# Performance work log

Measured on AMD Instinct MI355X. Metric: run time of the kernel, lower is better.

## Reference

```python
import jax, jax.numpy as jnp
import numpy as np

N_NODES = 20000
T_STEPS = 8


def _layer_norm(x, g, b, eps=1e-5):
    mu = x.mean(-1, keepdims=True)
    var = ((x - mu) ** 2).mean(-1, keepdims=True)
    return (x - mu) * jax.lax.rsqrt(var + eps) * g + b


def _linear(x, W, b):
    # torch nn.Linear: x @ W.T + b, W is [out, in]
    return x @ W.T + b


def _gcn_conv(xw, norm, src, dst, b, n):
    # xw: pre-transformed features [N, H]; symmetric-normalized aggregation
    msg = xw[src] * norm[:, None]
    return jax.ops.segment_sum(msg, dst, num_segments=n) + b


def setup_inputs() -> dict:
    key = jax.random.key(0)
    ks = jax.random.split(key, 16)
    N, T, K, E, D, H, M = N_NODES, T_STEPS, 4000, 400000, 128, 128, 16
    s = 0.05
    return {
        "node_t": jax.random.randint(ks[0], (T, K), 0, N),
        "edge_index_t": jax.random.randint(ks[1], (T, 2, E), 0, N),
        "m": M,
        "emb": jax.random.normal(ks[2], (N, D), jnp.float32) * s,
        "convW1": jax.random.normal(ks[3], (H, D), jnp.float32) * s,
        "convb1": jnp.zeros((H,), jnp.float32),
        "convW2": jax.random.normal(ks[4], (H, H), jnp.float32) * s,
        "convb2": jnp.zeros((H,), jnp.float32),
        "tn_g": jnp.ones((H,), jnp.float32),
        "tn_b": jnp.zeros((H,), jnp.float32),
        "tok_w1": jax.random.normal(ks[5], (M, M), jnp.float32) * s,
        "tok_b1": jnp.zeros((M,), jnp.float32),
        "tok_w2": jax.random.normal(ks[6], (M, M), jnp.float32) * s,
        "tok_b2": jnp.zeros((M,), jnp.float32),
        "cn_g": jnp.ones((H,), jnp.float32),
        "cn_b": jnp.zeros((H,), jnp.float32),
        "ch_w1": jax.random.normal(ks[7], (H, H), jnp.float32) * s,
        "ch_b1": jnp.zeros((H,), jnp.float32),
        "ch_w2": jax.random.normal(ks[8], (H, H), jnp.float32) * s,
        "ch_b2": jnp.zeros((H,), jnp.float32),
    }


def reference(node_t, edge_index_t, m, emb, convW1, convb1, convW2, convb2,
              tn_g, tn_b, tok_w1, tok_b1, tok_w2, tok_b2,
              cn_g, cn_b, ch_w1, ch_b1, ch_w2, ch_b2):
    N = emb.shape[0]
    H = convW1.shape[0]
    gelu = lambda x: jax.nn.gelu(x, approximate=False)

    def mixer(x):  # x: [N, m, H]
        y = _layer_norm(x, tn_g, tn_b)
        y = jnp.swapaxes(y, 1, 2)                 # [N, H, m]
        y = _linear(gelu(_linear(y, tok_w1, tok_b1)), tok_w2, tok_b2)
        x = x + jnp.swapaxes(y, 1, 2)
        z = _layer_norm(x, cn_g, cn_b)
        z = _linear(gelu(_linear(z, ch_w1, ch_b1)), ch_w2, ch_b2)
        return x + z

    # conv linear transforms are per-node dense and constant w.r.t. step input emb
    xw1 = emb @ convW1.T                          # [N, H]
    self_loop = jnp.arange(N)

    def step(x_m, xs):
        node_i, edge_i = xs                        # [K], [2, E]
        x_m_new = mixer(x_m)
        x_new = x_m_new.mean(axis=1)               # FinalProcessLayer, discrete
        # GCN with self-loops and symmetric normalization
        src = jnp.concatenate([edge_i[0], self_loop])
        dst = jnp.concatenate([edge_i[1], self_loop])
        deg = jax.ops.segment_sum(jnp.ones_like(src, jnp.float32), dst,
                                  num_segments=N)
        dinv = jax.lax.rsqrt(jnp.maximum(deg, 1.0))
        norm = dinv[src] * dinv[dst]
        h = _gcn_conv(xw1, norm, src, dst, convb1, N)
        h = jax.nn.relu(h)
        h = _gcn_conv(h @ convW2.T, norm, src, dst, convb2, N)
        # zero rows of nodes present at this timestep (boolean-mask scatter)
        h = h.at[node_i].set(0.0)
        # slide window
        x_m = jnp.concatenate([x_m[:, 1:, :], h[:, None, :]], axis=1)
        return x_m, x_new

    x_m0 = jnp.zeros((N, m, H), jnp.float32)
    _, outs = jax.lax.scan(step, x_m0, (node_t, edge_index_t))
    return outs  # [T, N, H]
```

## Files before the change

kernel.cpp:

```cpp
#include <hip/hip_runtime.h>
#include <hip/hip_bf16.h>
#include <cstdint>
#include <cstddef>

#define NN 20000
#define HH 128
#define MM 16
#define KK 4000
#define EE 400000

typedef __attribute__((ext_vector_type(16))) float f16v;
typedef __attribute__((ext_vector_type(8))) short short8;
typedef __attribute__((ext_vector_type(4))) float f32x4;
typedef __attribute__((ext_vector_type(4), may_alias)) float f4ma;
typedef __attribute__((ext_vector_type(2), may_alias)) float f2ma;

__device__ __forceinline__ float gelu_f(float x) {
  return 0.5f * x * (1.0f + erff(x * 0.70710678118654752440f));
}

__device__ __forceinline__ short f2bf(float f) {
  union { float f; unsigned u; } v; v.f = f;
  unsigned u = v.u;
  unsigned r = (u + 0x7FFFu + ((u >> 16) & 1u)) >> 16;
  return (short)r;
}
__device__ __forceinline__ float bf2f(unsigned short s) {
  union { unsigned u; float f; } v; v.u = ((unsigned)s) << 16; return v.f;
}


__global__ void zero2_kernel(int* __restrict__ a, int* __restrict__ b, int n) {
  int i = blockIdx.x * 256 + threadIdx.x;
  if (i < n) { a[i] = 0; b[i] = 0; }
}

__global__ void count_kernel(const int* __restrict__ dst, int* __restrict__ cnt, int n) {
  int e = blockIdx.x * 256 + threadIdx.x;
  if (e < n) atomicAdd(&cnt[dst[e]], 1);
}

__global__ void dinv_kernel(const int* __restrict__ cnt, float* __restrict__ dinv, int n) {
  int i = blockIdx.x * 256 + threadIdx.x;
  if (i < n) dinv[i] = rsqrtf((float)(cnt[i] + 1));
}

__global__ void scan_kernel(const int* __restrict__ cnt, int* __restrict__ offs, int n) {
  __shared__ int sh[1024];
  __shared__ int carry_s;
  int tid = threadIdx.x;
  if (tid == 0) carry_s = 0;
  __syncthreads();
  for (int base = 0; base < n; base += 1024) {
    int i = base + tid;
    int v = (i < n) ? cnt[i] : 0;
    sh[tid] = v;
    __syncthreads();
    for (int off = 1; off < 1024; off <<= 1) {
      int t = (tid >= off) ? sh[tid - off] : 0;
      __syncthreads();
      sh[tid] += t;
      __syncthreads();
    }
    int carry = carry_s;
    if (i < n) offs[i] = carry + sh[tid] - v;
    __syncthreads();
    if (tid == 1023) carry_s = carry + sh[1023];
    __syncthreads();
  }
  if (tid == 0) offs[n] = carry_s;
}

__global__ void fillcsr_kernel(const int* __restrict__ esrc, const int* __restrict__ edst,
                               const int* __restrict__ offs, int* __restrict__ cursor,
                               const float* __restrict__ dinv,
                               int* __restrict__ csrc, float* __restrict__ cnorm, int n) {
  int e = blockIdx.x * 256 + threadIdx.x;
  if (e < n) {
    int s = esrc[e], d = edst[e];
    int pos = offs[d] + atomicAdd(&cursor[d], 1);
    csrc[pos] = s;
    cnorm[pos] = dinv[s] * dinv[d];
  }
}

__global__ __launch_bounds__(128) void agg_kernel(const float* __restrict__ X,
    const int* __restrict__ csrc, const float* __restrict__ cnorm,
    const int* __restrict__ offs, const float* __restrict__ dinv,
    const float* __restrict__ bias, int relu, float* __restrict__ Y) {
  int i = blockIdx.x, c = threadIdx.x;
  float di = dinv[i];
  float acc = X[(size_t)i * HH + c] * di * di;
  int s = offs[i], e = offs[i + 1];
  for (int j = s; j < e; ++j) {
    acc += X[(size_t)csrc[j] * HH + c] * cnorm[j];
  }
  acc += bias[c];
  if (relu) acc = fmaxf(acc, 0.f);
  Y[(size_t)i * HH + c] = acc;
}

__global__ __launch_bounds__(128) void gemm128_kernel(const float* __restrict__ X,
    const float* __restrict__ W, float* __restrict__ Y, int nrows) {
  __shared__ float Ws[128 * 129];
  __shared__ float Xs[8 * 128];
  int tid = threadIdx.x;
  for (int idx = tid; idx < 16384; idx += 128) {
    int o = idx >> 7, k = idx & 127;
    Ws[o * 129 + k] = W[idx];
  }
  __syncthreads();
  for (int row0 = blockIdx.x * 8; row0 < nrows; row0 += gridDim.x * 8) {
    int nr = min(8, nrows - row0);
    for (int idx = tid; idx < nr * 128; idx += 128) Xs[idx] = X[(size_t)row0 * 128 + idx];
    __syncthreads();
    float acc[8] = {0, 0, 0, 0, 0, 0, 0, 0};
    for (int k = 0; k < 128; ++k) {
      float w = Ws[tid * 129 + k];
#pragma unroll
      for (int r = 0; r < 8; ++r) acc[r] += w * Xs[r * 128 + k];
    }
    for (int r = 0; r < nr; ++r) Y[(size_t)(row0 + r) * 128 + tid] = acc[r];
    __syncthreads();
  }
}

__global__ void mask_kernel(const int* __restrict__ nodes, float* __restrict__ H, int kn) {
  int idx = blockIdx.x * 256 + threadIdx.x;
  if (idx < kn * HH) {
    int j = idx >> 7, c = idx & 127;
    H[(size_t)nodes[j] * HH + c] = 0.f;
  }
}

__global__ void bcast_kernel(float* __restrict__ out, int total) {
  int idx = blockIdx.x * 256 + threadIdx.x + 128;
  if (idx < total) out[idx] = out[idx & 127];
}


__global__ __launch_bounds__(256) void mixer14_kernel(
    const float* __restrict__ hbufs,
    const float* __restrict__ tn_g, const float* __restrict__ tn_b,
    const float* __restrict__ tok_w1, const float* __restrict__ tok_b1,
    const float* __restrict__ tok_w2, const float* __restrict__ tok_b2,
    const float* __restrict__ cn_g, const float* __restrict__ cn_b,
    const float* __restrict__ ch_w1, const float* __restrict__ ch_b1,
    const float* __restrict__ ch_w2, const float* __restrict__ ch_b2,
    float* __restrict__ out, int total_items, int niter) {
  __shared__ __align__(16) float zw[64 * 132];
  __shared__ float fout[4 * 128];
  __shared__ float tg[128], tbv[128], cg[128], cbv[128], cb1v[128], cb2v[128];
  __shared__ float tw1s[256], tw2s[256], tb1s[16], tb2s[16];

  const int tid = threadIdx.x;
  const int lane = tid & 63;
  const int wv = tid >> 6;
  const int q = lane >> 4;
  const int h = lane & 15;

  if (tid < 128) {
    tg[tid] = tn_g[tid]; tbv[tid] = tn_b[tid];
    cg[tid] = cn_g[tid]; cbv[tid] = cn_b[tid];
    cb1v[tid] = ch_b1[tid]; cb2v[tid] = ch_b2[tid];
  }
  tw1s[tid] = tok_w1[tid];
  tw2s[tid] = tok_w2[tid];
  if (tid < 16) { tb1s[tid] = tok_b1[tid]; tb2s[tid] = tok_b2[tid]; }

  short8 wf1[4][2], wf2[4][2];
#pragma unroll
  for (int ks = 0; ks < 4; ++ks) {
#pragma unroll
    for (int j = 0; j < 2; ++j) {
      int o = (2 * wv + j) * 16 + h;
      int k0 = ks * 32 + q * 8;
      const float* s1 = ch_w1 + o * 128 + k0;
      const float* s2 = ch_w2 + o * 128 + k0;
      short8 p1, p2;
#pragma unroll
      for (int e = 0; e < 8; ++e) { p1[e] = f2bf(s1[e]); p2[e] = f2bf(s2[e]); }
      wf1[ks][j] = p1;
      wf2[ks][j] = p2;
    }
  }
  __syncthreads();

  const int lr = tid >> 2;
  const int lq = tid & 3;
  const int c2 = tid & 127;
  const int n0 = tid >> 7;

  for (int it = 0; it < niter; ++it) {
    const int item4 = it * gridDim.x + blockIdx.x;

    {
      const int n = lr >> 4, tok = lr & 15;
      const int item = item4 * 4 + n;
      const bool act = item < total_items;
      int t = 0, node = 0;
      if (act && item < 7 * NN) { t = item / NN + 1; node = item % NN; }
      int src_t = tok - (MM - t);
      f4ma x[8];
      if (act && src_t >= 0) {
        const float* hp = hbufs + ((size_t)src_t * NN + node) * HH + lq * 32;
#pragma unroll
        for (int j = 0; j < 8; ++j) x[j] = *(const f4ma*)(hp + 4 * j);
      } else {
#pragma unroll
        for (int j = 0; j < 8; ++j) x[j] = (f4ma){0.f, 0.f, 0.f, 0.f};
      }
      float s = 0.f, ss = 0.f;
#pragma unroll
      for (int j = 0; j < 8; ++j) {
        s += x[j].x + x[j].y + x[j].z + x[j].w;
        ss += x[j].x * x[j].x + x[j].y * x[j].y + x[j].z * x[j].z + x[j].w * x[j].w;
      }
      s += __shfl_xor(s, 1); ss += __shfl_xor(ss, 1);
      s += __shfl_xor(s, 2); ss += __shfl_xor(ss, 2);
      float mu = s * (1.f / 128.f);
      float var = fmaxf(ss * (1.f / 128.f) - mu * mu, 0.f);
      float rs = rsqrtf(var + 1e-5f);
#pragma unroll
      for (int j = 0; j < 8; ++j) *(f4ma*)&zw[lr * 132 + lq * 32 + 4 * j] = x[j];
      if (lq == 0) { zw[lr * 132 + 128] = mu; zw[lr * 132 + 129] = rs; }
    }
    __syncthreads();

    {
      const int rb0 = n0 * 16 * 132, rb1 = (n0 + 2) * 16 * 132;
      const float tgc = tg[c2], tbc = tbv[c2];
      f16v xv0, xv1, zv0, zv1;
#pragma unroll
      for (int r = 0; r < 16; ++r) {
        float x0 = zw[rb0 + r * 132 + c2];
        float m0 = zw[rb0 + r * 132 + 128], q0 = zw[rb0 + r * 132 + 129];
        float x1 = zw[rb1 + r * 132 + c2];
        float m1 = zw[rb1 + r * 132 + 128], q1 = zw[rb1 + r * 132 + 129];
        xv0[r] = x0; xv1[r] = x1;
        zv0[r] = (x0 - m0) * q0 * tgc + tbc;
        zv1[r] = (x1 - m1) * q1 * tgc + tbc;
      }
      f16v a0v, a1v;
#pragma unroll
      for (int hd = 0; hd < 16; ++hd) {
        float acc0 = tb1s[hd], acc1 = tb1s[hd];
#pragma unroll
        for (int rq = 0; rq < 4; ++rq) {
          f4ma w = *(const f4ma*)&tw1s[hd * 16 + rq * 4];
          acc0 += w.x * zv0[rq * 4] + w.y * zv0[rq * 4 + 1] +
                  w.z * zv0[rq * 4 + 2] + w.w * zv0[rq * 4 + 3];
          acc1 += w.x * zv1[rq * 4] + w.y * zv1[rq * 4 + 1] +
                  w.z * zv1[rq * 4 + 2] + w.w * zv1[rq * 4 + 3];
        }
        a0v[hd] = gelu_f(acc0); a1v[hd] = gelu_f(acc1);
      }
      float cs0 = 0.f, cs1 = 0.f;
#pragma unroll
      for (int r = 0; r < 16; ++r) {
        float o0 = tb2s[r], o1 = tb2s[r];
#pragma unroll
        for (int hq = 0; hq < 4; ++hq) {
          f4ma w = *(const f4ma*)&tw2s[r * 16 + hq * 4];
          o0 += w.x * a0v[hq * 4] + w.y * a0v[hq * 4 + 1] +
                w.z * a0v[hq * 4 + 2] + w.w * a0v[hq * 4 + 3];
          o1 += w.x * a1v[hq * 4] + w.y * a1v[hq * 4 + 1] +
                w.z * a1v[hq * 4 + 2] + w.w * a1v[hq * 4 + 3];
        }
        float nx0 = xv0[r] + o0, nx1 = xv1[r] + o1;
        cs0 += nx0; cs1 += nx1;
        zw[rb0 + r * 132 + c2] = nx0;
        zw[rb1 + r * 132 + c2] = nx1;
      }
      fout[n0 * 128 + c2] = cs0;
      fout[(n0 + 2) * 128 + c2] = cs1;
    }
    __syncthreads();

    {
      f4ma x[8];
#pragma unroll
      for (int j = 0; j < 8; ++j) x[j] = *(const f4ma*)&zw[lr * 132 + lq * 32 + 4 * j];
      float s = 0.f, ss = 0.f;
#pragma unroll
      for (int j = 0; j < 8; ++j) {
        s += x[j].x + x[j].y + x[j].z + x[j].w;
        ss += x[j].x * x[j].x + x[j].y * x[j].y + x[j].z * x[j].z + x[j].w * x[j].w;
      }
      s += __shfl_xor(s, 1); ss += __shfl_xor(ss, 1);
      s += __shfl_xor(s, 2); ss += __shfl_xor(ss, 2);
      float mu = s * (1.f / 128.f);
      float var = fmaxf(ss * (1.f / 128.f) - mu * mu, 0.f);
      float rs = rsqrtf(var + 1e-5f);
#pragma unroll
      for (int j = 0; j < 8; ++j) {
        int c = lq * 32 + 4 * j;
        f4ma z;
        z.x = (x[j].x - mu) * rs * cg[c]     + cbv[c];
        z.y = (x[j].y - mu) * rs * cg[c + 1] + cbv[c + 1];
        z.z = (x[j].z - mu) * rs * cg[c + 2] + cbv[c + 2];
        z.w = (x[j].w - mu) * rs * cg[c + 3] + cbv[c + 3];
        *(f4ma*)&zw[lr * 132 + c] = z;
      }
    }
    __syncthreads();

    {
      f32x4 acc[4][2];
#pragma unroll
      for (int rt = 0; rt < 4; ++rt) {
#pragma unroll
        for (int j = 0; j < 2; ++j) {
          float b = cb1v[(2 * wv + j) * 16 + h];
          acc[rt][j] = (f32x4){b, b, b, b};
        }
      }
#pragma unroll
      for (int ks = 0; ks < 4; ++ks) {
        short8 ah[4], al[4];
#pragma unroll
        for (int rt = 0; rt < 4; ++rt) {
          f4ma v0 = *(const f4ma*)&zw[(rt * 16 + h) * 132 + ks * 32 + q * 8];
          f4ma v1 = *(const f4ma*)&zw[(rt * 16 + h) * 132 + ks * 32 + q * 8 + 4];
          float e[8] = {v0.x, v0.y, v0.z, v0.w, v1.x, v1.y, v1.z, v1.w};
          short8 th, tl;
#pragma unroll
          for (int j = 0; j < 8; ++j) {
            short hi = f2bf(e[j]);
            th[j] = hi;
            tl[j] = f2bf(e[j] - bf2f((unsigned short)hi));
          }
          ah[rt] = th; al[rt] = tl;
        }
#pragma unroll
        for (int rt = 0; rt < 4; ++rt) {
#pragma unroll
          for (int j = 0; j < 2; ++j) {
            acc[rt][j] = __builtin_amdgcn_mfma_f32_16x16x32_bf16(ah[rt], wf1[ks][j], acc[rt][j], 0, 0, 0);
            acc[rt][j] = __builtin_amdgcn_mfma_f32_16x16x32_bf16(al[rt], wf1[ks][j], acc[rt][j], 0, 0, 0);
          }
        }
      }
      __syncthreads();
#pragma unroll
      for (int rt = 0; rt < 4; ++rt) {
#pragma unroll
        for (int j = 0; j < 2; ++j) {
#pragma unroll
          for (int rg = 0; rg < 4; ++rg) {
            zw[(rt * 16 + q * 4 + rg) * 132 + (2 * wv + j) * 16 + h] = gelu_f(acc[rt][j][rg]);
          }
        }
      }
    }
    __syncthreads();

    {
      f32x4 acc[4][2];
#pragma unroll
      for (int rt = 0; rt < 4; ++rt) {
#pragma unroll
        for (int j = 0; j < 2; ++j) {
          float b = cb2v[(2 * wv + j) * 16 + h];
          acc[rt][j] = (f32x4){b, b, b, b};
        }
      }
#pragma unroll
      for (int ks = 0; ks < 4; ++ks) {
        short8 ah[4], al[4];
#pragma unroll
        for (int rt = 0; rt < 4; ++rt) {
          f4ma v0 = *(const f4ma*)&zw[(rt * 16 + h) * 132 + ks * 32 + q * 8];
          f4ma v1 = *(const f4ma*)&zw[(rt * 16 + h) * 132 + ks * 32 + q * 8 + 4];
          float e[8] = {v0.x, v0.y, v0.z, v0.w, v1.x, v1.y, v1.z, v1.w};
          short8 th, tl;
#pragma unroll
          for (int j = 0; j < 8; ++j) {
            short hi = f2bf(e[j]);
            th[j] = hi;
            tl[j] = f2bf(e[j] - bf2f((unsigned short)hi));
          }
          ah[rt] = th; al[rt] = tl;
        }
#pragma unroll
        for (int rt = 0; rt < 4; ++rt) {
#pragma unroll
          for (int j = 0; j < 2; ++j) {
            acc[rt][j] = __builtin_amdgcn_mfma_f32_16x16x32_bf16(ah[rt], wf2[ks][j], acc[rt][j], 0, 0, 0);
            acc[rt][j] = __builtin_amdgcn_mfma_f32_16x16x32_bf16(al[rt], wf2[ks][j], acc[rt][j], 0, 0, 0);
          }
        }
      }
#pragma unroll
      for (int rt = 0; rt < 4; ++rt) {
        const int item = item4 * 4 + rt;
        const bool act = item < total_items;
        int t = 0, node = 0;
        if (act && item < 7 * NN) { t = item / NN + 1; node = item % NN; }
#pragma unroll
        for (int j = 0; j < 2; ++j) {
          float v = acc[rt][j][0] + acc[rt][j][1] + acc[rt][j][2] + acc[rt][j][3];
          v += __shfl_xor(v, 16);
          v += __shfl_xor(v, 32);
          if (q == 0 && act) {
            int col = (2 * wv + j) * 16 + h;
            out[((size_t)t * NN + node) * HH + col] = (fout[rt * 128 + col] + v) * (1.f / 16.f);
          }
        }
      }
    }
    __syncthreads();
  }
}


extern "C" void kernel_launch(void* const* d_in, const int* in_sizes, int n_in,
                              void* d_out, int out_size, void* d_ws, size_t ws_size,
                              hipStream_t stream) {
  const int* node_t   = (const int*)d_in[0];
  const int* edges    = (const int*)d_in[1];
  const float* emb    = (const float*)d_in[3];
  const float* convW1 = (const float*)d_in[4];
  const float* convb1 = (const float*)d_in[5];
  const float* convW2 = (const float*)d_in[6];
  const float* convb2 = (const float*)d_in[7];
  const float* tn_g   = (const float*)d_in[8];
  const float* tn_b   = (const float*)d_in[9];
  const float* tok_w1 = (const float*)d_in[10];
  const float* tok_b1 = (const float*)d_in[11];
  const float* tok_w2 = (const float*)d_in[12];
  const float* tok_b2 = (const float*)d_in[13];
  const float* cn_g   = (const float*)d_in[14];
  const float* cn_b   = (const float*)d_in[15];
  const float* ch_w1  = (const float*)d_in[16];
  const float* ch_b1  = (const float*)d_in[17];
  const float* ch_w2  = (const float*)d_in[18];
  const float* ch_b2  = (const float*)d_in[19];
  float* out = (float*)d_out;

  char* ws = (char*)d_ws;
  size_t off = 0;
  auto alloc = [&](size_t bytes) -> void* {
    void* p = ws + off;
    off += (bytes + 511) & ~(size_t)511;
    return p;
  };
  float* xw1   = (float*)alloc((size_t)NN * HH * 4);
  float* hbufs = (float*)alloc((size_t)7 * NN * HH * 4);
  float* h     = (float*)alloc((size_t)NN * HH * 4);
  float* h2    = (float*)alloc((size_t)NN * HH * 4);
  float* dinv  = (float*)alloc((size_t)NN * 4);
  int*   cnt   = (int*)alloc((size_t)NN * 4);
  int*   cursor= (int*)alloc((size_t)NN * 4);
  int*   offs  = (int*)alloc((size_t)(NN + 1) * 4);
  int*   csrc  = (int*)alloc((size_t)EE * 4);
  float* cnorm = (float*)alloc((size_t)EE * 4);

  gemm128_kernel<<<512, 128, 0, stream>>>(emb, convW1, xw1, NN);

  for (int t = 0; t < 7; ++t) {
    const int* es = edges + (size_t)t * 2 * EE;
    const int* ed = es + EE;
    zero2_kernel<<<(NN + 255) / 256, 256, 0, stream>>>(cnt, cursor, NN);
    count_kernel<<<(EE + 255) / 256, 256, 0, stream>>>(ed, cnt, EE);
    dinv_kernel<<<(NN + 255) / 256, 256, 0, stream>>>(cnt, dinv, NN);
    scan_kernel<<<1, 1024, 0, stream>>>(cnt, offs, NN);
    fillcsr_kernel<<<(EE + 255) / 256, 256, 0, stream>>>(es, ed, offs, cursor, dinv,
                                                         csrc, cnorm, EE);
    agg_kernel<<<NN, 128, 0, stream>>>(xw1, csrc, cnorm, offs, dinv, convb1, 1, h);
    gemm128_kernel<<<512, 128, 0, stream>>>(h, convW2, h2, NN);
    agg_kernel<<<NN, 128, 0, stream>>>(h2, csrc, cnorm, offs, dinv, convb2, 0,
                                       hbufs + (size_t)t * NN * HH);
    mask_kernel<<<(KK * HH + 255) / 256, 256, 0, stream>>>(
        node_t + (size_t)t * KK, hbufs + (size_t)t * NN * HH, KK);
  }

  const int total_items = 7 * NN + 1;
  const int nblocks = 2048;
  const int item4s = (total_items + 3) / 4;
  const int niter = (item4s + nblocks - 1) / nblocks;
  mixer14_kernel<<<nblocks, 256, 0, stream>>>(hbufs, tn_g, tn_b, tok_w1, tok_b1, tok_w2,
                                              tok_b2, cn_g, cn_b, ch_w1, ch_b1, ch_w2,
                                              ch_b2, out, total_items, niter);
  bcast_kernel<<<((NN * HH - 128) + 255) / 256, 256, 0, stream>>>(out, NN * HH);
}
```

Measured before the change: 3.939 ms.

## Stage bf16 hi/lo split operands in swizzled LDS for channel-mixer MFMAs

The mixer kernel now converts the layer-normed and GELU activations to bf16 hi/lo pairs once when it writes them, storing them in two new XOR-swizzled shared arrays. The MFMA loops then load short8 fragments directly instead of reading fp32 and splitting per fragment. The token-mixing loops are restructured into an outer-product accumulation that drops the per-row register arrays, and launch bounds request two blocks per CU. This raises LDS use by about 35KB per block, which may limit occupancy.

```diff
diff --git a/kernel.cpp b/kernel.cpp
--- a/kernel.cpp
+++ b/kernel.cpp
@@ -12,18 +12,18 @@
 typedef __attribute__((ext_vector_type(16))) float f16v;
 typedef __attribute__((ext_vector_type(8))) short short8;
 typedef __attribute__((ext_vector_type(4))) float f32x4;
+typedef __attribute__((ext_vector_type(8), may_alias)) short s8ma;
 typedef __attribute__((ext_vector_type(4), may_alias)) float f4ma;
-typedef __attribute__((ext_vector_type(2), may_alias)) float f2ma;
 
 __device__ __forceinline__ float gelu_f(float x) {
   return 0.5f * x * (1.0f + erff(x * 0.70710678118654752440f));
 }
 
-__device__ __forceinline__ short f2bf(float f) {
+__device__ __forceinline__ unsigned short f2bf(float f) {
   union { float f; unsigned u; } v; v.f = f;
   unsigned u = v.u;
   unsigned r = (u + 0x7FFFu + ((u >> 16) & 1u)) >> 16;
-  return (short)r;
+  return (unsigned short)r;
 }
 __device__ __forceinline__ float bf2f(unsigned short s) {
   union { unsigned u; float f; } v; v.u = ((unsigned)s) << 16; return v.f;
@@ -139,7 +139,7 @@
 }
 
 
-__global__ __launch_bounds__(256) void mixer14_kernel(
+__global__ __launch_bounds__(256, 2) void mixer15_kernel(
     const float* __restrict__ hbufs,
     const float* __restrict__ tn_g, const float* __restrict__ tn_b,
     const float* __restrict__ tok_w1, const float* __restrict__ tok_b1,
@@ -149,6 +149,8 @@
     const float* __restrict__ ch_w2, const float* __restrict__ ch_b2,
     float* __restrict__ out, int total_items, int niter) {
   __shared__ __align__(16) float zw[64 * 132];
+  __shared__ __align__(16) unsigned short zh[64 * 136];
+  __shared__ __align__(16) unsigned short zl[64 * 136];
   __shared__ float fout[4 * 128];
   __shared__ float tg[128], tbv[128], cg[128], cbv[128], cb1v[128], cb2v[128];
   __shared__ float tw1s[256], tw2s[256], tb1s[16], tb2s[16];
@@ -179,7 +181,7 @@
       const float* s2 = ch_w2 + o * 128 + k0;
       short8 p1, p2;
 #pragma unroll
-      for (int e = 0; e < 8; ++e) { p1[e] = f2bf(s1[e]); p2[e] = f2bf(s2[e]); }
+      for (int e = 0; e < 8; ++e) { p1[e] = (short)f2bf(s1[e]); p2[e] = (short)f2bf(s2[e]); }
       wf1[ks][j] = p1;
       wf2[ks][j] = p2;
     }
@@ -230,44 +232,36 @@
     {
       const int rb0 = n0 * 16 * 132, rb1 = (n0 + 2) * 16 * 132;
       const float tgc = tg[c2], tbc = tbv[c2];
-      f16v xv0, xv1, zv0, zv1;
+      f16v a0v, a1v;
+#pragma unroll
+      for (int hd = 0; hd < 16; ++hd) { float b = tb1s[hd]; a0v[hd] = b; a1v[hd] = b; }
 #pragma unroll
       for (int r = 0; r < 16; ++r) {
         float x0 = zw[rb0 + r * 132 + c2];
         float m0 = zw[rb0 + r * 132 + 128], q0 = zw[rb0 + r * 132 + 129];
         float x1 = zw[rb1 + r * 132 + c2];
         float m1 = zw[rb1 + r * 132 + 128], q1 = zw[rb1 + r * 132 + 129];
-        xv0[r] = x0; xv1[r] = x1;
-        zv0[r] = (x0 - m0) * q0 * tgc + tbc;
-        zv1[r] = (x1 - m1) * q1 * tgc + tbc;
-      }
-      f16v a0v, a1v;
-#pragma unroll
-      for (int hd = 0; hd < 16; ++hd) {
-        float acc0 = tb1s[hd], acc1 = tb1s[hd];
-#pragma unroll
-        for (int rq = 0; rq < 4; ++rq) {
-          f4ma w = *(const f4ma*)&tw1s[hd * 16 + rq * 4];
-          acc0 += w.x * zv0[rq * 4] + w.y * zv0[rq * 4 + 1] +
-                  w.z * zv0[rq * 4 + 2] + w.w * zv0[rq * 4 + 3];
-          acc1 += w.x * zv1[rq * 4] + w.y * zv1[rq * 4 + 1] +
-                  w.z * zv1[rq * 4 + 2] + w.w * zv1[rq * 4 + 3];
-        }
-        a0v[hd] = gelu_f(acc0); a1v[hd] = gelu_f(acc1);
-      }
+        float z0 = (x0 - m0) * q0 * tgc + tbc;
+        float z1 = (x1 - m1) * q1 * tgc + tbc;
+#pragma unroll
+        for (int hd = 0; hd < 16; ++hd) {
+          float w = tw1s[hd * 16 + r];
+          a0v[hd] += w * z0; a1v[hd] += w * z1;
+        }
+      }
+#pragma unroll
+      for (int hd = 0; hd < 16; ++hd) { a0v[hd] = gelu_f(a0v[hd]); a1v[hd] = gelu_f(a1v[hd]); }
       float cs0 = 0.f, cs1 = 0.f;
 #pragma unroll
       for (int r = 0; r < 16; ++r) {
         float o0 = tb2s[r], o1 = tb2s[r];
 #pragma unroll
-        for (int hq = 0; hq < 4; ++hq) {
-          f4ma w = *(const f4ma*)&tw2s[r * 16 + hq * 4];
-          o0 += w.x * a0v[hq * 4] + w.y * a0v[hq * 4 + 1] +
-                w.z * a0v[hq * 4 + 2] + w.w * a0v[hq * 4 + 3];
-          o1 += w.x * a1v[hq * 4] + w.y * a1v[hq * 4 + 1] +
-                w.z * a1v[hq * 4 + 2] + w.w * a1v[hq * 4 + 3];
-        }
-        float nx0 = xv0[r] + o0, nx1 = xv1[r] + o1;
+        for (int hd = 0; hd < 16; ++hd) {
+          float w = tw2s[r * 16 + hd];
+          o0 += w * a0v[hd]; o1 += w * a1v[hd];
+        }
+        float nx0 = zw[rb0 + r * 132 + c2] + o0;
+        float nx1 = zw[rb1 + r * 132 + c2] + o1;
         cs0 += nx0; cs1 += nx1;
         zw[rb0 + r * 132 + c2] = nx0;
         zw[rb1 + r * 132 + c2] = nx1;
@@ -292,15 +286,23 @@
       float mu = s * (1.f / 128.f);
       float var = fmaxf(ss * (1.f / 128.f) - mu * mu, 0.f);
       float rs = rsqrtf(var + 1e-5f);
-#pragma unroll
-      for (int j = 0; j < 8; ++j) {
-        int c = lq * 32 + 4 * j;
-        f4ma z;
-        z.x = (x[j].x - mu) * rs * cg[c]     + cbv[c];
-        z.y = (x[j].y - mu) * rs * cg[c + 1] + cbv[c + 1];
-        z.z = (x[j].z - mu) * rs * cg[c + 2] + cbv[c + 2];
-        z.w = (x[j].w - mu) * rs * cg[c + 3] + cbv[c + 3];
-        *(f4ma*)&zw[lr * 132 + c] = z;
+      const int sw = ((lr & 7) << 3);
+#pragma unroll
+      for (int j = 0; j < 4; ++j) {
+        int c0 = lq * 32 + 8 * j;
+        short8 ph, pl;
+#pragma unroll
+        for (int e = 0; e < 8; ++e) {
+          int c = c0 + e;
+          float zf = (((e < 4) ? ((const float*)&x[2 * j])[e] :
+                                 ((const float*)&x[2 * j + 1])[e - 4]) - mu) * rs * cg[c] + cbv[c];
+          unsigned short hi = f2bf(zf);
+          ph[e] = (short)hi;
+          pl[e] = (short)f2bf(zf - bf2f(hi));
+        }
+        int scol = c0 ^ sw;
+        *(s8ma*)&zh[lr * 136 + scol] = (s8ma)ph;
+        *(s8ma*)&zl[lr * 136 + scol] = (s8ma)pl;
       }
     }
     __syncthreads();
@@ -315,30 +317,19 @@
           acc[rt][j] = (f32x4){b, b, b, b};
         }
       }
+      const int sw = ((h & 7) << 3);
 #pragma unroll
       for (int ks = 0; ks < 4; ++ks) {
-        short8 ah[4], al[4];
+        const int scol = (ks * 32 + q * 8) ^ sw;
 #pragma unroll
         for (int rt = 0; rt < 4; ++rt) {
-          f4ma v0 = *(const f4ma*)&zw[(rt * 16 + h) * 132 + ks * 32 + q * 8];
-          f4ma v1 = *(const f4ma*)&zw[(rt * 16 + h) * 132 + ks * 32 + q * 8 + 4];
-          float e[8] = {v0.x, v0.y, v0.z, v0.w, v1.x, v1.y, v1.z, v1.w};
-          short8 th, tl;
-#pragma unroll
-          for (int j = 0; j < 8; ++j) {
-            short hi = f2bf(e[j]);
-            th[j] = hi;
-            tl[j] = f2bf(e[j] - bf2f((unsigned short)hi));
+          short8 ah = (short8)(*(const s8ma*)&zh[(rt * 16 + h) * 136 + scol]);
+          short8 al = (short8)(*(const s8ma*)&zl[(rt * 16 + h) * 136 + scol]);
+#pragma unroll
+          for (int j = 0; j < 2; ++j) {
+            acc[rt][j] = __builtin_amdgcn_mfma_f32_16x16x32_bf16(ah, wf1[ks][j], acc[rt][j], 0, 0, 0);
+            acc[rt][j] = __builtin_amdgcn_mfma_f32_16x16x32_bf16(al, wf1[ks][j], acc[rt][j], 0, 0, 0);
           }
-          ah[rt] = th; al[rt] = tl;
-        }
-#pragma unroll
-        for (int rt = 0; rt < 4; ++rt) {
-#pragma unroll
-          for (int j = 0; j < 2; ++j) {
-            acc[rt][j] = __builtin_amdgcn_mfma_f32_16x16x32_bf16(ah[rt], wf1[ks][j], acc[rt][j], 0, 0, 0);
-            acc[rt][j] = __builtin_amdgcn_mfma_f32_16x16x32_bf16(al[rt], wf1[ks][j], acc[rt][j], 0, 0, 0);
-          }
         }
       }
       __syncthreads();
@@ -346,9 +337,15 @@
       for (int rt = 0; rt < 4; ++rt) {
 #pragma unroll
         for (int j = 0; j < 2; ++j) {
+          int col = (2 * wv + j) * 16 + h;
 #pragma unroll
           for (int rg = 0; rg < 4; ++rg) {
-            zw[(rt * 16 + q * 4 + rg) * 132 + (2 * wv + j) * 16 + h] = gelu_f(acc[rt][j][rg]);
+            int row = rt * 16 + q * 4 + rg;
+            float v = gelu_f(acc[rt][j][rg]);
+            unsigned short hi = f2bf(v);
+            int scol = col ^ ((row & 7) << 3);
+            zh[row * 136 + scol] = hi;
+            zl[row * 136 + scol] = f2bf(v - bf2f(hi));
           }
         }
       }
@@ -365,29 +362,18 @@
           acc[rt][j] = (f32x4){b, b, b, b};
         }
       }
+      const int sw = ((h & 7) << 3);
 #pragma unroll
       for (int ks = 0; ks < 4; ++ks) {
-        short8 ah[4], al[4];
+        const int scol = (ks * 32 + q * 8) ^ sw;
 #pragma unroll
         for (int rt = 0; rt < 4; ++rt) {
-          f4ma v0 = *(const f4ma*)&zw[(rt * 16 + h) * 132 + ks * 32 + q * 8];
-          f4ma v1 = *(const f4ma*)&zw[(rt * 16 + h) * 132 + ks * 32 + q * 8 + 4];
-          float e[8] = {v0.x, v0.y, v0.z, v0.w, v1.x, v1.y, v1.z, v1.w};
-          short8 th, tl;
-#pragma unroll
-          for (int j = 0; j < 8; ++j) {
-            short hi = f2bf(e[j]);
-            th[j] = hi;
-            tl[j] = f2bf(e[j] - bf2f((unsigned short)hi));
-          }
-          ah[rt] = th; al[rt] = tl;
-        }
-#pragma unroll
-        for (int rt = 0; rt < 4; ++rt) {
+          short8 ah = (short8)(*(const s8ma*)&zh[(rt * 16 + h) * 136 + scol]);
+          short8 al = (short8)(*(const s8ma*)&zl[(rt * 16 + h) * 136 + scol]);
 #pragma unroll
           for (int j = 0; j < 2; ++j) {
-            acc[rt][j] = __builtin_amdgcn_mfma_f32_16x16x32_bf16(ah[rt], wf2[ks][j], acc[rt][j], 0, 0, 0);
-            acc[rt][j] = __builtin_amdgcn_mfma_f32_16x16x32_bf16(al[rt], wf2[ks][j], acc[rt][j], 0, 0, 0);
+            acc[rt][j] = __builtin_amdgcn_mfma_f32_16x16x32_bf16(ah, wf2[ks][j], acc[rt][j], 0, 0, 0);
+            acc[rt][j] = __builtin_amdgcn_mfma_f32_16x16x32_bf16(al, wf2[ks][j], acc[rt][j], 0, 0, 0);
           }
         }
       }
@@ -479,7 +465,7 @@
   const int nblocks = 2048;
   const int item4s = (total_items + 3) / 4;
   const int niter = (item4s + nblocks - 1) / nblocks;
-  mixer14_kernel<<<nblocks, 256, 0, stream>>>(hbufs, tn_g, tn_b, tok_w1, tok_b1, tok_w2,
+  mixer15_kernel<<<nblocks, 256, 0, stream>>>(hbufs, tn_g, tn_b, tok_w1, tok_b1, tok_w2,
                                               tok_b2, cn_g, cn_b, ch_w1, ch_b1, ch_w2,
                                               ch_b2, out, total_items, niter);
   bcast_kernel<<<((NN * HH - 128) + 255) / 256, 256, 0, stream>>>(out, NN * HH);
```

After: 6.224 ms. 1.58x slower.
